# Performance work log

Measured on AMD Instinct MI355X. Metric: run time of the kernel, lower is better.

Reference implementation:

```python
import jax, jax.numpy as jnp
import numpy as np


def _mlp(h, W_in, b_in, W_hid, b_hid, W_out, b_out):
    # 392 -> 1000 -> (1000)x4 -> 392, ReLU between linear layers (NICE shift net)
    h = jax.nn.relu(h @ W_in + b_in)
    for i in range(W_hid.shape[0]):  # fixed small layer count, not a data dim
        h = jax.nn.relu(h @ W_hid[i] + b_hid[i])
    return h @ W_out + b_out


def setup_inputs() -> dict:
    key = jax.random.key(0)
    ks = jax.random.split(key, 4)
    B, D, MID = 4096, 784, 1000
    half = D // 2
    return {
        "x": jax.random.normal(ks[0], (B, D), jnp.float32),
        "log_det_J": jnp.zeros((1,), jnp.float32),
        "W_in": jax.random.normal(ks[1], (half, MID), jnp.float32) * 0.05,
        "b_in": jnp.zeros((MID,), jnp.float32),
        "W_hid": jax.random.normal(ks[2], (4, MID, MID), jnp.float32) * 0.03,
        "b_hid": jnp.zeros((4, MID), jnp.float32),
        "W_out": jax.random.normal(ks[3], (MID, half), jnp.float32) * 0.03,
        "b_out": jnp.zeros((half,), jnp.float32),
    }


def reference(x, log_det_J, W_in, b_in, W_hid, b_hid, W_out, b_out):
    # mask_config = 0: first = even columns, second = odd columns
    first = x[:, 0::2]   # (B, D/2)
    second = x[:, 1::2]  # (B, D/2)
    shift = _mlp(first, W_in, b_in, W_hid, b_hid, W_out, b_out)
    y_second = second + shift  # coupling_law (reverse=False)
    # interleave: y[:, 0::2] = first, y[:, 1::2] = y_second, in one strided write
    y = jnp.stack([first, y_second], axis=2).reshape(x.shape)
    return (y, log_det_J)
```

## Files before the change

### kernel.cpp

```cpp
#include <hip/hip_runtime.h>

typedef __bf16 bf16;
typedef __bf16 bf16x8 __attribute__((ext_vector_type(8)));
typedef float f32x4 __attribute__((ext_vector_type(4)));

#define M_TOT 4096
#define D_IN  784
#define HALF  392
#define MID   1000
#define K0PAD 448
#define NPAD  1024

__device__ __forceinline__ void g2l16(const bf16* g, bf16* l) {
  __builtin_amdgcn_global_load_lds(
      (__attribute__((address_space(1))) void*)(g),
      (__attribute__((address_space(3))) void*)(l),
      16, 0, 0);
}

__global__ void prep_k(const float* __restrict__ x, const float* __restrict__ ldj,
                       const float* __restrict__ W_in, const float* __restrict__ W_hid,
                       const float* __restrict__ W_out,
                       bf16* __restrict__ A0, bf16* __restrict__ WT0,
                       bf16* __restrict__ WTh, bf16* __restrict__ WT5,
                       float* __restrict__ y) {
  int b = blockIdx.x;
  int tid = threadIdx.x;
  if (b == 0 && tid == 0) y[(size_t)M_TOT * D_IN] = ldj[0];

  if (b < 8192) {
    int m = b >> 1;
    int k = (b & 1) * 256 + tid;
    if (k < K0PAD)
      A0[(size_t)m * K0PAD + k] = (k < HALF) ? (bf16)x[(size_t)m * D_IN + 2 * k] : (bf16)0.f;
    return;
  }
  int t = b - 8192;
  const float* W; bf16* WT; int K, N, Kpad, tn, tk;
  if (t < 448) {
    W = W_in; WT = WT0; K = HALF; N = MID; Kpad = K0PAD;
    tn = t & 31; tk = t >> 5;
  } else if (t < 448 + 4096) {
    int u = t - 448; int i = u >> 10; u &= 1023;
    W = W_hid + (size_t)i * MID * MID; WT = WTh + (size_t)i * NPAD * NPAD;
    K = MID; N = MID; Kpad = NPAD;
    tn = u & 31; tk = u >> 5;
  } else {
    int u = t - 4544;
    W = W_out; WT = WT5; K = MID; N = HALF; Kpad = NPAD;
    tn = u & 15; tk = u >> 4;
  }
  __shared__ float tb[32][33];
  int n0 = tn * 32, k0 = tk * 32;
  int tx = tid & 31, ty = tid >> 5;
#pragma unroll
  for (int r = 0; r < 4; ++r) {
    int k = k0 + ty + 8 * r, n = n0 + tx;
    tb[ty + 8 * r][tx] = (k < K && n < N) ? W[(size_t)k * N + n] : 0.f;
  }
  __syncthreads();
#pragma unroll
  for (int r = 0; r < 4; ++r) {
    int n = n0 + ty + 8 * r, k = k0 + tx;
    WT[(size_t)n * Kpad + k] = (bf16)tb[tx][ty + 8 * r];
  }
}

template <int BM, int BN, int EPI, int K>
__global__ __launch_bounds__(256, 2)
void gemm_k(const bf16* __restrict__ A, const bf16* __restrict__ BT,
            const float* __restrict__ bias, int bias_n,
            bf16* __restrict__ C,
            const float* __restrict__ x, float* __restrict__ y) {
  constexpr int BK = 64;
  constexpr int MT = BM / 32, NT = BN / 32;
  constexpr int KT = K / BK;
  __shared__ bf16 ldsA[2][BM * BK];
  __shared__ bf16 ldsB[2][BN * BK];
  const int tid = threadIdx.x, wave = tid >> 6, lane = tid & 63;
  const int bm = blockIdx.x, bn = blockIdx.y;

  const int srow = lane >> 3;
  const int sq = (lane & 7) ^ srow;
  const bf16* gA = A + ((size_t)bm * BM + wave * (BM / 4) + srow) * K + sq * 8;
  const bf16* gB = BT + ((size_t)bn * BN + wave * (BN / 4) + srow) * K + sq * 8;
  const int lAoff = wave * (BM / 4) * BK;
  const int lBoff = wave * (BN / 4) * BK;

  const int mlane = lane & 15, quad = lane >> 4;
  const int wm = (wave & 1) * (BM / 2), wn = (wave >> 1) * (BN / 2);
  const int axor = mlane & 7;

  f32x4 acc[MT][NT] = {};

#pragma unroll
  for (int i = 0; i < BM / 32; ++i) g2l16(gA + (size_t)(8 * i) * K, &ldsA[0][lAoff + (8 * i) * BK]);
#pragma unroll
  for (int i = 0; i < BN / 32; ++i) g2l16(gB + (size_t)(8 * i) * K, &ldsB[0][lBoff + (8 * i) * BK]);

  for (int kt = 0; kt < KT; ++kt) {
    const int cur = kt & 1, nxt = cur ^ 1;
    __syncthreads();
    if (kt + 1 < KT) {
      const size_t off = (size_t)(kt + 1) * BK;
#pragma unroll
      for (int i = 0; i < BM / 32; ++i) g2l16(gA + off + (size_t)(8 * i) * K, &ldsA[nxt][lAoff + (8 * i) * BK]);
#pragma unroll
      for (int i = 0; i < BN / 32; ++i) g2l16(gB + off + (size_t)(8 * i) * K, &ldsB[nxt][lBoff + (8 * i) * BK]);
    }
    const bf16* raBase = &ldsA[cur][(wm + mlane) * BK];
    const bf16* rbBase = &ldsB[cur][(wn + mlane) * BK];
    bf16x8 af[2][MT], bfr[2][NT];
#pragma unroll
    for (int s = 0; s < 2; ++s) {
      const int co = ((s * 4 + quad) ^ axor) * 8;
#pragma unroll
      for (int i = 0; i < MT; ++i) af[s][i] = *(const bf16x8*)(raBase + i * 16 * BK + co);
#pragma unroll
      for (int i = 0; i < NT; ++i) bfr[s][i] = *(const bf16x8*)(rbBase + i * 16 * BK + co);
    }
#pragma unroll
    for (int s = 0; s < 2; ++s)
#pragma unroll
      for (int mt = 0; mt < MT; ++mt)
#pragma unroll
        for (int nt = 0; nt < NT; ++nt)
          acc[mt][nt] = __builtin_amdgcn_mfma_f32_16x16x32_bf16(
              af[s][mt], bfr[s][nt], acc[mt][nt], 0, 0, 0);
  }

  const int ng0 = bn * BN + wn + mlane;
  const int mg0 = bm * BM + wm + quad * 4;

  if (EPI == 0) {
    float bv[NT];
#pragma unroll
    for (int nt = 0; nt < NT; ++nt) {
      int n = ng0 + nt * 16;
      bv[nt] = (n < bias_n) ? bias[n] : 0.f;
    }
#pragma unroll
    for (int mt = 0; mt < MT; ++mt)
#pragma unroll
      for (int nt = 0; nt < NT; ++nt)
#pragma unroll
        for (int r = 0; r < 4; ++r) {
          int m = mg0 + mt * 16 + r;
          int n = ng0 + nt * 16;
          float v = fmaxf(acc[mt][nt][r] + bv[nt], 0.f);
          C[(size_t)m * NPAD + n] = (bf16)v;
        }
  } else {
    const float2* x2 = (const float2*)x;
    float2* y2 = (float2*)y;
#pragma unroll
    for (int nt = 0; nt < NT; ++nt) {
      int n = ng0 + nt * 16;
      if (n < HALF) {
        float bb = bias[n];
#pragma unroll
        for (int mt = 0; mt < MT; ++mt)
#pragma unroll
          for (int r = 0; r < 4; ++r) {
            int m = mg0 + mt * 16 + r;
            size_t off = (size_t)m * (D_IN / 2) + n;
            float2 v = x2[off];
            v.y += acc[mt][nt][r] + bb;
            y2[off] = v;
          }
      }
    }
  }
}

extern "C" void kernel_launch(void* const* d_in, const int* in_sizes, int n_in,
                              void* d_out, int out_size, void* d_ws, size_t ws_size,
                              hipStream_t stream) {
  const float* x     = (const float*)d_in[0];
  const float* ldj   = (const float*)d_in[1];
  const float* W_in  = (const float*)d_in[2];
  const float* b_in  = (const float*)d_in[3];
  const float* W_hid = (const float*)d_in[4];
  const float* b_hid = (const float*)d_in[5];
  const float* W_out = (const float*)d_in[6];
  const float* b_out = (const float*)d_in[7];
  float* y = (float*)d_out;

  char* p = (char*)d_ws;
  bf16* A0  = (bf16*)(p + 0);
  bf16* H0  = (bf16*)(p + 3670016);
  bf16* H1  = (bf16*)(p + 12058624);
  bf16* WT0 = (bf16*)(p + 20447232);
  bf16* WTh = (bf16*)(p + 21364736);
  bf16* WT5 = (bf16*)(p + 29753344);

  prep_k<<<dim3(8192 + 5056), 256, 0, stream>>>(x, ldj, W_in, W_hid, W_out,
                                                A0, WT0, WTh, WT5, y);

  gemm_k<64, 128, 0, K0PAD><<<dim3(64, 8), 256, 0, stream>>>(A0, WT0, b_in, MID, H0, nullptr, nullptr);
  gemm_k<64, 128, 0, NPAD><<<dim3(64, 8), 256, 0, stream>>>(H0, WTh + 0 * (size_t)NPAD * NPAD, b_hid + 0 * MID, MID, H1, nullptr, nullptr);
  gemm_k<64, 128, 0, NPAD><<<dim3(64, 8), 256, 0, stream>>>(H1, WTh + 1 * (size_t)NPAD * NPAD, b_hid + 1 * MID, MID, H0, nullptr, nullptr);
  gemm_k<64, 128, 0, NPAD><<<dim3(64, 8), 256, 0, stream>>>(H0, WTh + 2 * (size_t)NPAD * NPAD, b_hid + 2 * MID, MID, H1, nullptr, nullptr);
  gemm_k<64, 128, 0, NPAD><<<dim3(64, 8), 256, 0, stream>>>(H1, WTh + 3 * (size_t)NPAD * NPAD, b_hid + 3 * MID, MID, H0, nullptr, nullptr);
  gemm_k<64, 64, 1, NPAD><<<dim3(64, 8), 256, 0, stream>>>(H0, WT5, b_out, HALF, nullptr, x, y);
}
```

Measured before the change: 195.2 us.

## Replace LDS-staged double-buffered GEMM tiles with direct global fragment loads

Removes the shared-memory staging (global_load_lds double buffering, barriers, XOR swizzle) from the GEMM kernel. Each wave now loads its MFMA A/B fragments straight from global memory into registers. This drops the LDS traffic and per-iteration barriers, but loses sharing of tiles across waves, so global/L2 traffic rises and there is no explicit prefetch overlap.

New measurement: 327.8 us. 1.68x slower.

```diff
diff --git a/kernel.cpp b/kernel.cpp
--- a/kernel.cpp
+++ b/kernel.cpp
@@ -10,13 +10,6 @@
 #define MID   1000
 #define K0PAD 448
 #define NPAD  1024
-
-__device__ __forceinline__ void g2l16(const bf16* g, bf16* l) {
-  __builtin_amdgcn_global_load_lds(
-      (__attribute__((address_space(1))) void*)(g),
-      (__attribute__((address_space(3))) void*)(l),
-      16, 0, 0);
-}
 
 __global__ void prep_k(const float* __restrict__ x, const float* __restrict__ ldj,
                        const float* __restrict__ W_in, const float* __restrict__ W_hid,
@@ -66,58 +59,42 @@
   }
 }
 
-template <int BM, int BN, int EPI, int K>
+template <int BN, int EPI, int K>
 __global__ __launch_bounds__(256, 2)
 void gemm_k(const bf16* __restrict__ A, const bf16* __restrict__ BT,
             const float* __restrict__ bias, int bias_n,
             bf16* __restrict__ C,
             const float* __restrict__ x, float* __restrict__ y) {
-  constexpr int BK = 64;
-  constexpr int MT = BM / 32, NT = BN / 32;
-  constexpr int KT = K / BK;
-  __shared__ bf16 ldsA[2][BM * BK];
-  __shared__ bf16 ldsB[2][BN * BK];
+  constexpr int MT = 2, NT = BN / 32;
+  constexpr int KT = K / 64;
   const int tid = threadIdx.x, wave = tid >> 6, lane = tid & 63;
   const int bm = blockIdx.x, bn = blockIdx.y;
+  const int mlane = lane & 15, quad = lane >> 4;
+  const int wm = (wave & 1) * 32, wn = (wave >> 1) * (BN / 2);
+  const int kq = quad * 8;
 
-  const int srow = lane >> 3;
-  const int sq = (lane & 7) ^ srow;
-  const bf16* gA = A + ((size_t)bm * BM + wave * (BM / 4) + srow) * K + sq * 8;
-  const bf16* gB = BT + ((size_t)bn * BN + wave * (BN / 4) + srow) * K + sq * 8;
-  const int lAoff = wave * (BM / 4) * BK;
-  const int lBoff = wave * (BN / 4) * BK;
-
-  const int mlane = lane & 15, quad = lane >> 4;
-  const int wm = (wave & 1) * (BM / 2), wn = (wave >> 1) * (BN / 2);
-  const int axor = mlane & 7;
+  const bf16* pa[MT];
+  const bf16* pb[NT];
+#pragma unroll
+  for (int mt = 0; mt < MT; ++mt)
+    pa[mt] = A + (size_t)(bm * 64 + wm + mt * 16 + mlane) * K + kq;
+#pragma unroll
+  for (int nt = 0; nt < NT; ++nt)
+    pb[nt] = BT + (size_t)(bn * BN + wn + nt * 16 + mlane) * K + kq;
 
   f32x4 acc[MT][NT] = {};
 
 #pragma unroll
-  for (int i = 0; i < BM / 32; ++i) g2l16(gA + (size_t)(8 * i) * K, &ldsA[0][lAoff + (8 * i) * BK]);
-#pragma unroll
-  for (int i = 0; i < BN / 32; ++i) g2l16(gB + (size_t)(8 * i) * K, &ldsB[0][lBoff + (8 * i) * BK]);
-
   for (int kt = 0; kt < KT; ++kt) {
-    const int cur = kt & 1, nxt = cur ^ 1;
-    __syncthreads();
-    if (kt + 1 < KT) {
-      const size_t off = (size_t)(kt + 1) * BK;
-#pragma unroll
-      for (int i = 0; i < BM / 32; ++i) g2l16(gA + off + (size_t)(8 * i) * K, &ldsA[nxt][lAoff + (8 * i) * BK]);
-#pragma unroll
-      for (int i = 0; i < BN / 32; ++i) g2l16(gB + off + (size_t)(8 * i) * K, &ldsB[nxt][lBoff + (8 * i) * BK]);
-    }
-    const bf16* raBase = &ldsA[cur][(wm + mlane) * BK];
-    const bf16* rbBase = &ldsB[cur][(wn + mlane) * BK];
     bf16x8 af[2][MT], bfr[2][NT];
 #pragma unroll
     for (int s = 0; s < 2; ++s) {
-      const int co = ((s * 4 + quad) ^ axor) * 8;
 #pragma unroll
-      for (int i = 0; i < MT; ++i) af[s][i] = *(const bf16x8*)(raBase + i * 16 * BK + co);
+      for (int mt = 0; mt < MT; ++mt)
+        af[s][mt] = *(const bf16x8*)(pa[mt] + kt * 64 + s * 32);
 #pragma unroll
-      for (int i = 0; i < NT; ++i) bfr[s][i] = *(const bf16x8*)(rbBase + i * 16 * BK + co);
+      for (int nt = 0; nt < NT; ++nt)
+        bfr[s][nt] = *(const bf16x8*)(pb[nt] + kt * 64 + s * 32);
     }
 #pragma unroll
     for (int s = 0; s < 2; ++s)
@@ -130,7 +107,7 @@
   }
 
   const int ng0 = bn * BN + wn + mlane;
-  const int mg0 = bm * BM + wm + quad * 4;
+  const int mg0 = bm * 64 + wm + quad * 4;
 
   if (EPI == 0) {
     float bv[NT];
@@ -197,10 +174,10 @@
   prep_k<<<dim3(8192 + 5056), 256, 0, stream>>>(x, ldj, W_in, W_hid, W_out,
                                                 A0, WT0, WTh, WT5, y);
 
-  gemm_k<64, 128, 0, K0PAD><<<dim3(64, 8), 256, 0, stream>>>(A0, WT0, b_in, MID, H0, nullptr, nullptr);
-  gemm_k<64, 128, 0, NPAD><<<dim3(64, 8), 256, 0, stream>>>(H0, WTh + 0 * (size_t)NPAD * NPAD, b_hid + 0 * MID, MID, H1, nullptr, nullptr);
-  gemm_k<64, 128, 0, NPAD><<<dim3(64, 8), 256, 0, stream>>>(H1, WTh + 1 * (size_t)NPAD * NPAD, b_hid + 1 * MID, MID, H0, nullptr, nullptr);
-  gemm_k<64, 128, 0, NPAD><<<dim3(64, 8), 256, 0, stream>>>(H0, WTh + 2 * (size_t)NPAD * NPAD, b_hid + 2 * MID, MID, H1, nullptr, nullptr);
-  gemm_k<64, 128, 0, NPAD><<<dim3(64, 8), 256, 0, stream>>>(H1, WTh + 3 * (size_t)NPAD * NPAD, b_hid + 3 * MID, MID, H0, nullptr, nullptr);
-  gemm_k<64, 64, 1, NPAD><<<dim3(64, 8), 256, 0, stream>>>(H0, WT5, b_out, HALF, nullptr, x, y);
+  gemm_k<128, 0, K0PAD><<<dim3(64, 8), 256, 0, stream>>>(A0, WT0, b_in, MID, H0, nullptr, nullptr);
+  gemm_k<128, 0, NPAD><<<dim3(64, 8), 256, 0, stream>>>(H0, WTh + 0 * (size_t)NPAD * NPAD, b_hid + 0 * MID, MID, H1, nullptr, nullptr);
+  gemm_k<128, 0, NPAD><<<dim3(64, 8), 256, 0, stream>>>(H1, WTh + 1 * (size_t)NPAD * NPAD, b_hid + 1 * MID, MID, H0, nullptr, nullptr);
+  gemm_k<128, 0, NPAD><<<dim3(64, 8), 256, 0, stream>>>(H0, WTh + 2 * (size_t)NPAD * NPAD, b_hid + 2 * MID, MID, H1, nullptr, nullptr);
+  gemm_k<128, 0, NPAD><<<dim3(64, 8), 256, 0, stream>>>(H1, WTh + 3 * (size_t)NPAD * NPAD, b_hid + 3 * MID, MID, H0, nullptr, nullptr);
+  gemm_k<64, 1, NPAD><<<dim3(64, 8), 256, 0, stream>>>(H0, WT5, b_out, HALF, nullptr, x, y);
 }
```
